# Performance work log

Measured on AMD Instinct MI355X. Metric: run time of the kernel, lower is better.

The kernel has to match this reference:

```python
import jax, jax.numpy as jnp
import numpy as np

C = 32          # mid_channel / in_channel
B = 8           # batch size (number of scenes)
N = 2_000_000   # total points across batch
BN_EPS = 1e-4   # BatchNorm1d eps from norm_fn


def setup_inputs() -> dict:
    key = jax.random.key(0)
    ks = jax.random.split(key, 8)
    s = 0.05
    return {
        "feats": jax.random.normal(ks[0], (N, C), dtype=jnp.float32),
        "batch_idxs": jnp.sort(jax.random.randint(ks[1], (N,), 0, B, dtype=jnp.int32)),
        "off_w1": jax.random.normal(ks[2], (C, C), dtype=jnp.float32) * s,
        "off_b1": jnp.zeros((C,), jnp.float32),
        "bn_gamma": jnp.ones((C,), jnp.float32),   # set_bn_init fills 1.0
        "bn_beta": jnp.zeros((C,), jnp.float32),   # set_bn_init fills 0.0
        "off_w2": jax.random.normal(ks[3], (C, 3), dtype=jnp.float32) * s,
        "off_b2": jnp.zeros((3,), jnp.float32),
        "mask_w1": jax.random.normal(ks[4], (C, C), dtype=jnp.float32) * s,
        "mask_b1": jnp.zeros((C,), jnp.float32),
        "mask_w2": jax.random.normal(ks[5], (C, 1), dtype=jnp.float32) * s,
        "mask_b2": jnp.zeros((1,), jnp.float32),
        "iou_w": jax.random.normal(ks[6], (C, 1), dtype=jnp.float32) * s,
        "iou_b": jnp.zeros((1,), jnp.float32),
    }


def reference(feats, batch_idxs, off_w1, off_b1, bn_gamma, bn_beta, off_w2, off_b2,
              mask_w1, mask_b1, mask_w2, mask_b2, iou_w, iou_b):
    # offset_linear = MLP([C, C, 3], norm_fn=BatchNorm1d): Linear -> BN -> ReLU -> Linear
    h = feats @ off_w1 + off_b1                      # [N, C]
    mu = h.mean(axis=0)
    var = jnp.mean(jnp.square(h - mu), axis=0)       # biased var (torch BN training fwd)
    h = (h - mu) * jax.lax.rsqrt(var + BN_EPS) * bn_gamma + bn_beta
    h = jax.nn.relu(h)
    pt_offsets = h @ off_w2 + off_b2                 # [N, 3]

    # mask_linear = MLP([C, C, 1], norm_fn=None): Linear -> ReLU -> Linear
    m = jax.nn.relu(feats @ mask_w1 + mask_b1)       # [N, C]
    mask_scores = m @ mask_w2 + mask_b2              # [N, 1]

    # global_pool: scatter mean of features over per-batch segments (batch offsets)
    ones = jnp.ones((feats.shape[0],), feats.dtype)
    counts = jax.ops.segment_sum(ones, batch_idxs, num_segments=B)          # [B]
    pooled = jax.ops.segment_sum(feats, batch_idxs, num_segments=B)         # [B, C]
    pooled = pooled / jnp.maximum(counts, 1.0)[:, None]

    # iou_score_linear on the pooled proposal feature
    iou_scores = pooled @ iou_w + iou_b              # [B, 1]
    return pt_offsets, mask_scores, pooled, iou_scores
```

## Files before the change

kernel.cpp:

```cpp
#include <hip/hip_runtime.h>

#define TPB 256
#define NBLK 1024

typedef __attribute__((ext_vector_type(8))) short short8;
typedef __attribute__((ext_vector_type(4))) float floatx4;

__device__ __forceinline__ unsigned short bf_trunc(float f){
    union { float f; unsigned u; } c; c.f = f;
    return (unsigned short)(c.u >> 16);
}
__device__ __forceinline__ unsigned short bf_rne(float f){
    union { float f; unsigned u; } c; c.f = f;
    unsigned r = c.u + 0x7fffu + ((c.u >> 16) & 1u);
    return (unsigned short)(r >> 16);
}

__global__ __launch_bounds__(TPB) void pass1_kernel(
    const float* __restrict__ feats, const int* __restrict__ bidx,
    const float* __restrict__ w1, const float* __restrict__ b1,
    const float* __restrict__ mw1, const float* __restrict__ mb1,
    const float* __restrict__ mw2, const float* __restrict__ mb2,
    float* __restrict__ mask_out,
    float* __restrict__ ws_sum, float* __restrict__ ws_sq,
    float* __restrict__ ws_pool, int N)
{
    __shared__ float s_pool[8][32];
    __shared__ float s_sum[32];
    __shared__ float s_sq[32];

    const int tid = threadIdx.x;
    if (tid < 32){ s_sum[tid] = 0.f; s_sq[tid] = 0.f; }
    ((float*)s_pool)[tid] = 0.f;
    __syncthreads();

    const int lane = tid & 63;
    const int p = lane & 15;
    const int q = lane >> 4;

    short8 aw0, aw1, am0, am1;
    floatx4 ci_h0, ci_h1, ci_m0, ci_m1;
    float mw2v[8];
#pragma unroll
    for (int j = 0; j < 8; ++j){
        const int k = q * 8 + j;
        aw0[j] = (short)bf_rne(w1 [k * 32 + p]);
        aw1[j] = (short)bf_rne(w1 [k * 32 + 16 + p]);
        am0[j] = (short)bf_rne(mw1[k * 32 + p]);
        am1[j] = (short)bf_rne(mw1[k * 32 + 16 + p]);
    }
#pragma unroll
    for (int r = 0; r < 4; ++r){
        const int c0 = q * 4 + r, c1 = 16 + q * 4 + r;
        ci_h0[r] = b1[c0];  ci_h1[r] = b1[c1];
        ci_m0[r] = mb1[c0]; ci_m1[r] = mb1[c1];
        mw2v[r] = mw2[c0];  mw2v[4 + r] = mw2[c1];
    }
    const float mb2s = mb2[0];

    float hsum[8] = {0,0,0,0,0,0,0,0};
    float hsq [8] = {0,0,0,0,0,0,0,0};
    float pacc[8] = {0,0,0,0,0,0,0,0};
    int curb = -1;

    const int  ntiles = (N + 15) >> 4;
    const long nw  = (long)gridDim.x * (TPB / 64);
    const long wid = (long)blockIdx.x * (TPB / 64) + (tid >> 6);
    const int  t0 = (int)(wid * (long)ntiles / nw);
    const int  t1 = (int)((wid + 1) * (long)ntiles / nw);

    for (int t = t0; t < t1; ++t){
        const int row0 = t << 4;
        const int row  = row0 + p;
        const bool valid = (row < N);

        floatx4 v0 = {0.f,0.f,0.f,0.f}, v1 = {0.f,0.f,0.f,0.f};
        if (valid){
            const floatx4* rp = (const floatx4*)(feats + (size_t)row * 32 + q * 8);
            v0 = rp[0]; v1 = rp[1];
        }

        const int b = valid ? bidx[row] : -1;
        if (b != curb){
            if (curb >= 0){
#pragma unroll
                for (int j = 0; j < 8; ++j){
                    atomicAdd(&s_pool[curb][q * 8 + j], pacc[j]);
                    pacc[j] = 0.f;
                }
            }
            curb = b;
        }
        if (b >= 0){
            pacc[0] += v0[0]; pacc[1] += v0[1]; pacc[2] += v0[2]; pacc[3] += v0[3];
            pacc[4] += v1[0]; pacc[5] += v1[1]; pacc[6] += v1[2]; pacc[7] += v1[3];
        }

        short8 bfrag;
        bfrag[0] = (short)bf_trunc(v0[0]); bfrag[1] = (short)bf_trunc(v0[1]);
        bfrag[2] = (short)bf_trunc(v0[2]); bfrag[3] = (short)bf_trunc(v0[3]);
        bfrag[4] = (short)bf_trunc(v1[0]); bfrag[5] = (short)bf_trunc(v1[1]);
        bfrag[6] = (short)bf_trunc(v1[2]); bfrag[7] = (short)bf_trunc(v1[3]);

        const floatx4 ch0 = __builtin_amdgcn_mfma_f32_16x16x32_bf16(aw0, bfrag, ci_h0, 0, 0, 0);
        const floatx4 ch1 = __builtin_amdgcn_mfma_f32_16x16x32_bf16(aw1, bfrag, ci_h1, 0, 0, 0);
        const floatx4 cm0 = __builtin_amdgcn_mfma_f32_16x16x32_bf16(am0, bfrag, ci_m0, 0, 0, 0);
        const floatx4 cm1 = __builtin_amdgcn_mfma_f32_16x16x32_bf16(am1, bfrag, ci_m1, 0, 0, 0);

        if (valid){
#pragma unroll
            for (int r = 0; r < 4; ++r){
                const float h0 = ch0[r]; hsum[r]     += h0; hsq[r]     = fmaf(h0, h0, hsq[r]);
                const float h1 = ch1[r]; hsum[4 + r] += h1; hsq[4 + r] = fmaf(h1, h1, hsq[4 + r]);
            }
        }

        float tm = 0.f;
#pragma unroll
        for (int r = 0; r < 4; ++r){
            tm = fmaf(fmaxf(cm0[r], 0.f), mw2v[r],     tm);
            tm = fmaf(fmaxf(cm1[r], 0.f), mw2v[4 + r], tm);
        }
        tm += __shfl_xor(tm, 16, 64);
        tm += __shfl_xor(tm, 32, 64);
        if (q == 0 && valid) mask_out[row] = tm + mb2s;
    }

    if (curb >= 0){
#pragma unroll
        for (int j = 0; j < 8; ++j) atomicAdd(&s_pool[curb][q * 8 + j], pacc[j]);
    }
#pragma unroll
    for (int i = 0; i < 8; ++i){
        const int ch = (i >> 2) * 16 + q * 4 + (i & 3);
        atomicAdd(&s_sum[ch], hsum[i]);
        atomicAdd(&s_sq[ch],  hsq[i]);
    }
    __syncthreads();
    if (tid < 32){
        atomicAdd(&ws_sum[tid], s_sum[tid]);
        atomicAdd(&ws_sq[tid],  s_sq[tid]);
    }
    {
        const float pv = ((float*)s_pool)[tid];
        if (pv != 0.f) atomicAdd(&ws_pool[tid], pv);
    }
}

__global__ __launch_bounds__(TPB) void finalize_kernel(
    const int* __restrict__ bidx,
    const float* __restrict__ gamma, const float* __restrict__ beta,
    const float* __restrict__ w1, const float* __restrict__ b1,
    const float* __restrict__ iw, const float* __restrict__ ib,
    const float* __restrict__ ws_sum, const float* __restrict__ ws_sq,
    const float* __restrict__ ws_pool,
    float* __restrict__ ws_w1f, float* __restrict__ ws_b1f,
    float* __restrict__ pooled_out, float* __restrict__ iou_out,
    int N, int B)
{
    __shared__ float s_s[32];
    __shared__ float s_pooled[256];
    __shared__ int   s_lb[33];

    const int tid = threadIdx.x;
    if (tid <= B){
        int lo = 0, hi = N;
        while (lo < hi){
            const int mid = (lo + hi) >> 1;
            if (bidx[mid] < tid) lo = mid + 1; else hi = mid;
        }
        s_lb[tid] = lo;
    }
    if (tid < 32){
        const float invN = 1.f / (float)N;
        const float mu  = ws_sum[tid] * invN;
        const float var = ws_sq[tid] * invN - mu * mu;
        const float s   = gamma[tid] * rsqrtf(var + 1e-4f);
        s_s[tid] = s;
        ws_b1f[tid] = (b1[tid] - mu) * s + beta[tid];
    }
    __syncthreads();
    for (int idx = tid; idx < 1024; idx += TPB)
        ws_w1f[idx] = w1[idx] * s_s[idx & 31];
    if (tid < B * 32){
        const int b = tid >> 5;
        const float cnt = fmaxf((float)(s_lb[b + 1] - s_lb[b]), 1.f);
        const float p = ws_pool[tid] / cnt;
        s_pooled[tid]   = p;
        pooled_out[tid] = p;
    }
    __syncthreads();
    if (tid < B){
        float acc = ib[0];
#pragma unroll
        for (int i = 0; i < 32; ++i) acc = fmaf(s_pooled[tid * 32 + i], iw[i], acc);
        iou_out[tid] = acc;
    }
}

__global__ __launch_bounds__(TPB) void pass2_kernel(
    const float* __restrict__ feats,
    const float* __restrict__ ws_w1f, const float* __restrict__ ws_b1f,
    const float* __restrict__ w2, const float* __restrict__ b2,
    float* __restrict__ pt_out, int N)
{
    const int tid = threadIdx.x;
    const int lane = tid & 63;
    const int p = lane & 15;
    const int q = lane >> 4;

    short8 aw0, aw1;
    floatx4 ci0, ci1;
    float w2v[24];
    float b2v0, b2v1, b2v2;
#pragma unroll
    for (int j = 0; j < 8; ++j){
        const int k = q * 8 + j;
        aw0[j] = (short)bf_rne(ws_w1f[k * 32 + p]);
        aw1[j] = (short)bf_rne(ws_w1f[k * 32 + 16 + p]);
    }
#pragma unroll
    for (int r = 0; r < 4; ++r){
        ci0[r] = ws_b1f[q * 4 + r];
        ci1[r] = ws_b1f[16 + q * 4 + r];
    }
#pragma unroll
    for (int i = 0; i < 8; ++i){
        const int ch = (i >> 2) * 16 + q * 4 + (i & 3);
        w2v[i]      = w2[ch * 3 + 0];
        w2v[8 + i]  = w2[ch * 3 + 1];
        w2v[16 + i] = w2[ch * 3 + 2];
    }
    b2v0 = b2[0]; b2v1 = b2[1]; b2v2 = b2[2];

    const int  ntiles = (N + 15) >> 4;
    const long nw  = (long)gridDim.x * (TPB / 64);
    const long wid = (long)blockIdx.x * (TPB / 64) + (tid >> 6);
    const int  t0 = (int)(wid * (long)ntiles / nw);
    const int  t1 = (int)((wid + 1) * (long)ntiles / nw);

    for (int t = t0; t < t1; ++t){
        const int row0 = t << 4;
        const int row  = row0 + p;
        const bool valid = (row < N);

        floatx4 v0 = {0.f,0.f,0.f,0.f}, v1 = {0.f,0.f,0.f,0.f};
        if (valid){
            const floatx4* rp = (const floatx4*)(feats + (size_t)row * 32 + q * 8);
            v0 = rp[0]; v1 = rp[1];
        }
        short8 bfrag;
        bfrag[0] = (short)bf_trunc(v0[0]); bfrag[1] = (short)bf_trunc(v0[1]);
        bfrag[2] = (short)bf_trunc(v0[2]); bfrag[3] = (short)bf_trunc(v0[3]);
        bfrag[4] = (short)bf_trunc(v1[0]); bfrag[5] = (short)bf_trunc(v1[1]);
        bfrag[6] = (short)bf_trunc(v1[2]); bfrag[7] = (short)bf_trunc(v1[3]);

        const floatx4 c0 = __builtin_amdgcn_mfma_f32_16x16x32_bf16(aw0, bfrag, ci0, 0, 0, 0);
        const floatx4 c1 = __builtin_amdgcn_mfma_f32_16x16x32_bf16(aw1, bfrag, ci1, 0, 0, 0);

        float s0 = 0.f, s1 = 0.f, s2 = 0.f;
#pragma unroll
        for (int r = 0; r < 4; ++r){
            const float p0 = fmaxf(c0[r], 0.f);
            const float p1 = fmaxf(c1[r], 0.f);
            s0 = fmaf(p0, w2v[r],          s0); s0 = fmaf(p1, w2v[4 + r],      s0);
            s1 = fmaf(p0, w2v[8 + r],      s1); s1 = fmaf(p1, w2v[12 + r],     s1);
            s2 = fmaf(p0, w2v[16 + r],     s2); s2 = fmaf(p1, w2v[20 + r],     s2);
        }
        s0 += __shfl_xor(s0, 16, 64); s0 += __shfl_xor(s0, 32, 64);
        s1 += __shfl_xor(s1, 16, 64); s1 += __shfl_xor(s1, 32, 64);
        s2 += __shfl_xor(s2, 16, 64); s2 += __shfl_xor(s2, 32, 64);

        if (lane < 48 && valid){
            float val = (q == 0) ? (s0 + b2v0) : ((q == 1) ? (s1 + b2v1) : (s2 + b2v2));
            pt_out[(size_t)row0 * 3 + p * 3 + q] = val;
        }
    }
}

extern "C" void kernel_launch(void* const* d_in, const int* in_sizes, int n_in,
                              void* d_out, int out_size, void* d_ws, size_t ws_size,
                              hipStream_t stream) {
    const float* feats = (const float*)d_in[0];
    const int*   bidx  = (const int*)d_in[1];
    const float* w1    = (const float*)d_in[2];
    const float* b1    = (const float*)d_in[3];
    const float* gamma = (const float*)d_in[4];
    const float* beta  = (const float*)d_in[5];
    const float* w2    = (const float*)d_in[6];
    const float* b2    = (const float*)d_in[7];
    const float* mw1   = (const float*)d_in[8];
    const float* mb1   = (const float*)d_in[9];
    const float* mw2   = (const float*)d_in[10];
    const float* mb2   = (const float*)d_in[11];
    const float* iw    = (const float*)d_in[12];
    const float* ib    = (const float*)d_in[13];

    const int N = in_sizes[0] / 32;
    const int B = (out_size - 4 * N) / 33;

    float* out    = (float*)d_out;
    float* pt     = out;
    float* mask   = out + (size_t)3 * N;
    float* pooled = out + (size_t)4 * N;
    float* iou    = pooled + (size_t)B * 32;

    float* ws      = (float*)d_ws;
    float* ws_sum  = ws;
    float* ws_sq   = ws + 32;
    float* ws_pool = ws + 64;
    float* ws_b1f  = ws + 64 + B * 32;
    float* ws_w1f  = ws + 96 + B * 32;

    hipMemsetAsync(ws, 0, (size_t)(64 + B * 32) * sizeof(float), stream);

    pass1_kernel<<<NBLK, TPB, 0, stream>>>(feats, bidx, w1, b1, mw1, mb1, mw2, mb2,
                                           mask, ws_sum, ws_sq, ws_pool, N);
    finalize_kernel<<<1, TPB, 0, stream>>>(bidx, gamma, beta, w1, b1, iw, ib,
                                           ws_sum, ws_sq, ws_pool,
                                           ws_w1f, ws_b1f, pooled, iou, N, B);
    pass2_kernel<<<NBLK, TPB, 0, stream>>>(feats, ws_w1f, ws_b1f, w2, b2, pt, N);
}
```

Measured before the change: 474.8 us.

## Fuse three passes into one cooperative kernel with grid-wide sync

```diff
diff --git a/kernel.cpp b/kernel.cpp
--- a/kernel.cpp
+++ b/kernel.cpp
@@ -1,7 +1,10 @@
 #include <hip/hip_runtime.h>
+#include <hip/hip_cooperative_groups.h>
+
+namespace cg = cooperative_groups;
 
 #define TPB 256
-#define NBLK 1024
+#define MAXBLK 1024
 
 typedef __attribute__((ext_vector_type(8))) short short8;
 typedef __attribute__((ext_vector_type(4))) float floatx4;
@@ -16,47 +19,59 @@
     return (unsigned short)(r >> 16);
 }
 
-__global__ __launch_bounds__(TPB) void pass1_kernel(
-    const float* __restrict__ feats, const int* __restrict__ bidx,
-    const float* __restrict__ w1, const float* __restrict__ b1,
-    const float* __restrict__ mw1, const float* __restrict__ mb1,
-    const float* __restrict__ mw2, const float* __restrict__ mb2,
-    float* __restrict__ mask_out,
-    float* __restrict__ ws_sum, float* __restrict__ ws_sq,
-    float* __restrict__ ws_pool, int N)
+struct Params {
+    const float* feats; const int* bidx;
+    const float* w1; const float* b1;
+    const float* gamma; const float* beta;
+    const float* w2; const float* b2;
+    const float* mw1; const float* mb1;
+    const float* mw2; const float* mb2;
+    const float* iw; const float* ib;
+    float* pt; float* mask; float* pooled; float* iou;
+    float* ws_sum; float* ws_sq; float* ws_pool;
+    int N; int B;
+};
+
+__global__ __launch_bounds__(TPB, 4) void inst_head_fused(Params P)
 {
     __shared__ float s_pool[8][32];
     __shared__ float s_sum[32];
     __shared__ float s_sq[32];
-
-    const int tid = threadIdx.x;
+    __shared__ float s_sc[32];
+    __shared__ float s_bp[32];
+    __shared__ float s_pooled[256];
+    __shared__ int   s_lb[33];
+
+    const int tid  = threadIdx.x;
+    const int lane = tid & 63;
+    const int p = lane & 15;
+    const int q = lane >> 4;
+
+    const int N = P.N, B = P.B;
+
     if (tid < 32){ s_sum[tid] = 0.f; s_sq[tid] = 0.f; }
     ((float*)s_pool)[tid] = 0.f;
     __syncthreads();
 
-    const int lane = tid & 63;
-    const int p = lane & 15;
-    const int q = lane >> 4;
-
     short8 aw0, aw1, am0, am1;
     floatx4 ci_h0, ci_h1, ci_m0, ci_m1;
     float mw2v[8];
 #pragma unroll
     for (int j = 0; j < 8; ++j){
         const int k = q * 8 + j;
-        aw0[j] = (short)bf_rne(w1 [k * 32 + p]);
-        aw1[j] = (short)bf_rne(w1 [k * 32 + 16 + p]);
-        am0[j] = (short)bf_rne(mw1[k * 32 + p]);
-        am1[j] = (short)bf_rne(mw1[k * 32 + 16 + p]);
+        aw0[j] = (short)bf_rne(P.w1 [k * 32 + p]);
+        aw1[j] = (short)bf_rne(P.w1 [k * 32 + 16 + p]);
+        am0[j] = (short)bf_rne(P.mw1[k * 32 + p]);
+        am1[j] = (short)bf_rne(P.mw1[k * 32 + 16 + p]);
     }
 #pragma unroll
     for (int r = 0; r < 4; ++r){
         const int c0 = q * 4 + r, c1 = 16 + q * 4 + r;
-        ci_h0[r] = b1[c0];  ci_h1[r] = b1[c1];
-        ci_m0[r] = mb1[c0]; ci_m1[r] = mb1[c1];
-        mw2v[r] = mw2[c0];  mw2v[4 + r] = mw2[c1];
-    }
-    const float mb2s = mb2[0];
+        ci_h0[r] = P.b1[c0];  ci_h1[r] = P.b1[c1];
+        ci_m0[r] = P.mb1[c0]; ci_m1[r] = P.mb1[c1];
+        mw2v[r] = P.mw2[c0];  mw2v[4 + r] = P.mw2[c1];
+    }
+    const float mb2s = P.mb2[0];
 
     float hsum[8] = {0,0,0,0,0,0,0,0};
     float hsq [8] = {0,0,0,0,0,0,0,0};
@@ -76,11 +91,11 @@
 
         floatx4 v0 = {0.f,0.f,0.f,0.f}, v1 = {0.f,0.f,0.f,0.f};
         if (valid){
-            const floatx4* rp = (const floatx4*)(feats + (size_t)row * 32 + q * 8);
+            const floatx4* rp = (const floatx4*)(P.feats + (size_t)row * 32 + q * 8);
             v0 = rp[0]; v1 = rp[1];
         }
 
-        const int b = valid ? bidx[row] : -1;
+        const int b = valid ? P.bidx[row] : -1;
         if (b != curb){
             if (curb >= 0){
 #pragma unroll
@@ -123,7 +138,7 @@
         }
         tm += __shfl_xor(tm, 16, 64);
         tm += __shfl_xor(tm, 32, 64);
-        if (q == 0 && valid) mask_out[row] = tm + mb2s;
+        if (q == 0 && valid) P.mask[row] = tm + mb2s;
     }
 
     if (curb >= 0){
@@ -138,106 +153,75 @@
     }
     __syncthreads();
     if (tid < 32){
-        atomicAdd(&ws_sum[tid], s_sum[tid]);
-        atomicAdd(&ws_sq[tid],  s_sq[tid]);
+        atomicAdd(&P.ws_sum[tid], s_sum[tid]);
+        atomicAdd(&P.ws_sq[tid],  s_sq[tid]);
     }
     {
         const float pv = ((float*)s_pool)[tid];
-        if (pv != 0.f) atomicAdd(&ws_pool[tid], pv);
-    }
-}
-
-__global__ __launch_bounds__(TPB) void finalize_kernel(
-    const int* __restrict__ bidx,
-    const float* __restrict__ gamma, const float* __restrict__ beta,
-    const float* __restrict__ w1, const float* __restrict__ b1,
-    const float* __restrict__ iw, const float* __restrict__ ib,
-    const float* __restrict__ ws_sum, const float* __restrict__ ws_sq,
-    const float* __restrict__ ws_pool,
-    float* __restrict__ ws_w1f, float* __restrict__ ws_b1f,
-    float* __restrict__ pooled_out, float* __restrict__ iou_out,
-    int N, int B)
-{
-    __shared__ float s_s[32];
-    __shared__ float s_pooled[256];
-    __shared__ int   s_lb[33];
-
-    const int tid = threadIdx.x;
-    if (tid <= B){
-        int lo = 0, hi = N;
-        while (lo < hi){
-            const int mid = (lo + hi) >> 1;
-            if (bidx[mid] < tid) lo = mid + 1; else hi = mid;
-        }
-        s_lb[tid] = lo;
-    }
+        if (pv != 0.f) atomicAdd(&P.ws_pool[tid], pv);
+    }
+
+    cg::this_grid().sync();
+
+    if (blockIdx.x == 0){
+        if (tid <= B){
+            int lo = 0, hi = N;
+            while (lo < hi){
+                const int mid = (lo + hi) >> 1;
+                if (P.bidx[mid] < tid) lo = mid + 1; else hi = mid;
+            }
+            s_lb[tid] = lo;
+        }
+        __syncthreads();
+        if (tid < B * 32){
+            const int bb = tid >> 5;
+            const float cnt = fmaxf((float)(s_lb[bb + 1] - s_lb[bb]), 1.f);
+            const float pv = P.ws_pool[tid] / cnt;
+            s_pooled[tid] = pv;
+            P.pooled[tid] = pv;
+        }
+        __syncthreads();
+        if (tid < B){
+            float acc = P.ib[0];
+#pragma unroll
+            for (int i = 0; i < 32; ++i) acc = fmaf(s_pooled[tid * 32 + i], P.iw[i], acc);
+            P.iou[tid] = acc;
+        }
+    }
+
     if (tid < 32){
         const float invN = 1.f / (float)N;
-        const float mu  = ws_sum[tid] * invN;
-        const float var = ws_sq[tid] * invN - mu * mu;
-        const float s   = gamma[tid] * rsqrtf(var + 1e-4f);
-        s_s[tid] = s;
-        ws_b1f[tid] = (b1[tid] - mu) * s + beta[tid];
+        const float mu  = P.ws_sum[tid] * invN;
+        const float var = P.ws_sq[tid] * invN - mu * mu;
+        const float s   = P.gamma[tid] * rsqrtf(var + 1e-4f);
+        s_sc[tid] = s;
+        s_bp[tid] = (P.b1[tid] - mu) * s + P.beta[tid];
     }
     __syncthreads();
-    for (int idx = tid; idx < 1024; idx += TPB)
-        ws_w1f[idx] = w1[idx] * s_s[idx & 31];
-    if (tid < B * 32){
-        const int b = tid >> 5;
-        const float cnt = fmaxf((float)(s_lb[b + 1] - s_lb[b]), 1.f);
-        const float p = ws_pool[tid] / cnt;
-        s_pooled[tid]   = p;
-        pooled_out[tid] = p;
-    }
-    __syncthreads();
-    if (tid < B){
-        float acc = ib[0];
-#pragma unroll
-        for (int i = 0; i < 32; ++i) acc = fmaf(s_pooled[tid * 32 + i], iw[i], acc);
-        iou_out[tid] = acc;
-    }
-}
-
-__global__ __launch_bounds__(TPB) void pass2_kernel(
-    const float* __restrict__ feats,
-    const float* __restrict__ ws_w1f, const float* __restrict__ ws_b1f,
-    const float* __restrict__ w2, const float* __restrict__ b2,
-    float* __restrict__ pt_out, int N)
-{
-    const int tid = threadIdx.x;
-    const int lane = tid & 63;
-    const int p = lane & 15;
-    const int q = lane >> 4;
-
-    short8 aw0, aw1;
-    floatx4 ci0, ci1;
+
+    short8 pw0, pw1;
+    floatx4 pc0, pc1;
     float w2v[24];
-    float b2v0, b2v1, b2v2;
+    const float sc0 = s_sc[p], sc1 = s_sc[16 + p];
 #pragma unroll
     for (int j = 0; j < 8; ++j){
         const int k = q * 8 + j;
-        aw0[j] = (short)bf_rne(ws_w1f[k * 32 + p]);
-        aw1[j] = (short)bf_rne(ws_w1f[k * 32 + 16 + p]);
+        pw0[j] = (short)bf_rne(P.w1[k * 32 + p]      * sc0);
+        pw1[j] = (short)bf_rne(P.w1[k * 32 + 16 + p] * sc1);
     }
 #pragma unroll
     for (int r = 0; r < 4; ++r){
-        ci0[r] = ws_b1f[q * 4 + r];
-        ci1[r] = ws_b1f[16 + q * 4 + r];
+        pc0[r] = s_bp[q * 4 + r];
+        pc1[r] = s_bp[16 + q * 4 + r];
     }
 #pragma unroll
     for (int i = 0; i < 8; ++i){
         const int ch = (i >> 2) * 16 + q * 4 + (i & 3);
-        w2v[i]      = w2[ch * 3 + 0];
-        w2v[8 + i]  = w2[ch * 3 + 1];
-        w2v[16 + i] = w2[ch * 3 + 2];
-    }
-    b2v0 = b2[0]; b2v1 = b2[1]; b2v2 = b2[2];
-
-    const int  ntiles = (N + 15) >> 4;
-    const long nw  = (long)gridDim.x * (TPB / 64);
-    const long wid = (long)blockIdx.x * (TPB / 64) + (tid >> 6);
-    const int  t0 = (int)(wid * (long)ntiles / nw);
-    const int  t1 = (int)((wid + 1) * (long)ntiles / nw);
+        w2v[i]      = P.w2[ch * 3 + 0];
+        w2v[8 + i]  = P.w2[ch * 3 + 1];
+        w2v[16 + i] = P.w2[ch * 3 + 2];
+    }
+    const float b2v0 = P.b2[0], b2v1 = P.b2[1], b2v2 = P.b2[2];
 
     for (int t = t0; t < t1; ++t){
         const int row0 = t << 4;
@@ -246,7 +230,7 @@
 
         floatx4 v0 = {0.f,0.f,0.f,0.f}, v1 = {0.f,0.f,0.f,0.f};
         if (valid){
-            const floatx4* rp = (const floatx4*)(feats + (size_t)row * 32 + q * 8);
+            const floatx4* rp = (const floatx4*)(P.feats + (size_t)row * 32 + q * 8);
             v0 = rp[0]; v1 = rp[1];
         }
         short8 bfrag;
@@ -255,17 +239,17 @@
         bfrag[4] = (short)bf_trunc(v1[0]); bfrag[5] = (short)bf_trunc(v1[1]);
         bfrag[6] = (short)bf_trunc(v1[2]); bfrag[7] = (short)bf_trunc(v1[3]);
 
-        const floatx4 c0 = __builtin_amdgcn_mfma_f32_16x16x32_bf16(aw0, bfrag, ci0, 0, 0, 0);
-        const floatx4 c1 = __builtin_amdgcn_mfma_f32_16x16x32_bf16(aw1, bfrag, ci1, 0, 0, 0);
+        const floatx4 c0 = __builtin_amdgcn_mfma_f32_16x16x32_bf16(pw0, bfrag, pc0, 0, 0, 0);
+        const floatx4 c1 = __builtin_amdgcn_mfma_f32_16x16x32_bf16(pw1, bfrag, pc1, 0, 0, 0);
 
         float s0 = 0.f, s1 = 0.f, s2 = 0.f;
 #pragma unroll
         for (int r = 0; r < 4; ++r){
             const float p0 = fmaxf(c0[r], 0.f);
             const float p1 = fmaxf(c1[r], 0.f);
-            s0 = fmaf(p0, w2v[r],          s0); s0 = fmaf(p1, w2v[4 + r],      s0);
-            s1 = fmaf(p0, w2v[8 + r],      s1); s1 = fmaf(p1, w2v[12 + r],     s1);
-            s2 = fmaf(p0, w2v[16 + r],     s2); s2 = fmaf(p1, w2v[20 + r],     s2);
+            s0 = fmaf(p0, w2v[r],      s0); s0 = fmaf(p1, w2v[4 + r],  s0);
+            s1 = fmaf(p0, w2v[8 + r],  s1); s1 = fmaf(p1, w2v[12 + r], s1);
+            s2 = fmaf(p0, w2v[16 + r], s2); s2 = fmaf(p1, w2v[20 + r], s2);
         }
         s0 += __shfl_xor(s0, 16, 64); s0 += __shfl_xor(s0, 32, 64);
         s1 += __shfl_xor(s1, 16, 64); s1 += __shfl_xor(s1, 32, 64);
@@ -273,7 +257,7 @@
 
         if (lane < 48 && valid){
             float val = (q == 0) ? (s0 + b2v0) : ((q == 1) ? (s1 + b2v1) : (s2 + b2v2));
-            pt_out[(size_t)row0 * 3 + p * 3 + q] = val;
+            P.pt[(size_t)row0 * 3 + p * 3 + q] = val;
         }
     }
 }
@@ -281,43 +265,50 @@
 extern "C" void kernel_launch(void* const* d_in, const int* in_sizes, int n_in,
                               void* d_out, int out_size, void* d_ws, size_t ws_size,
                               hipStream_t stream) {
-    const float* feats = (const float*)d_in[0];
-    const int*   bidx  = (const int*)d_in[1];
-    const float* w1    = (const float*)d_in[2];
-    const float* b1    = (const float*)d_in[3];
-    const float* gamma = (const float*)d_in[4];
-    const float* beta  = (const float*)d_in[5];
-    const float* w2    = (const float*)d_in[6];
-    const float* b2    = (const float*)d_in[7];
-    const float* mw1   = (const float*)d_in[8];
-    const float* mb1   = (const float*)d_in[9];
-    const float* mw2   = (const float*)d_in[10];
-    const float* mb2   = (const float*)d_in[11];
-    const float* iw    = (const float*)d_in[12];
-    const float* ib    = (const float*)d_in[13];
+    Params P;
+    P.feats = (const float*)d_in[0];
+    P.bidx  = (const int*)d_in[1];
+    P.w1    = (const float*)d_in[2];
+    P.b1    = (const float*)d_in[3];
+    P.gamma = (const float*)d_in[4];
+    P.beta  = (const float*)d_in[5];
+    P.w2    = (const float*)d_in[6];
+    P.b2    = (const float*)d_in[7];
+    P.mw1   = (const float*)d_in[8];
+    P.mb1   = (const float*)d_in[9];
+    P.mw2   = (const float*)d_in[10];
+    P.mb2   = (const float*)d_in[11];
+    P.iw    = (const float*)d_in[12];
+    P.ib    = (const float*)d_in[13];
 
     const int N = in_sizes[0] / 32;
     const int B = (out_size - 4 * N) / 33;
-
-    float* out    = (float*)d_out;
-    float* pt     = out;
-    float* mask   = out + (size_t)3 * N;
-    float* pooled = out + (size_t)4 * N;
-    float* iou    = pooled + (size_t)B * 32;
-
-    float* ws      = (float*)d_ws;
-    float* ws_sum  = ws;
-    float* ws_sq   = ws + 32;
-    float* ws_pool = ws + 64;
-    float* ws_b1f  = ws + 64 + B * 32;
-    float* ws_w1f  = ws + 96 + B * 32;
+    P.N = N; P.B = B;
+
+    float* out = (float*)d_out;
+    P.pt     = out;
+    P.mask   = out + (size_t)3 * N;
+    P.pooled = out + (size_t)4 * N;
+    P.iou    = P.pooled + (size_t)B * 32;
+
+    float* ws = (float*)d_ws;
+    P.ws_sum  = ws;
+    P.ws_sq   = ws + 32;
+    P.ws_pool = ws + 64;
 
     hipMemsetAsync(ws, 0, (size_t)(64 + B * 32) * sizeof(float), stream);
 
-    pass1_kernel<<<NBLK, TPB, 0, stream>>>(feats, bidx, w1, b1, mw1, mb1, mw2, mb2,
-                                           mask, ws_sum, ws_sq, ws_pool, N);
-    finalize_kernel<<<1, TPB, 0, stream>>>(bidx, gamma, beta, w1, b1, iw, ib,
-                                           ws_sum, ws_sq, ws_pool,
-                                           ws_w1f, ws_b1f, pooled, iou, N, B);
-    pass2_kernel<<<NBLK, TPB, 0, stream>>>(feats, ws_w1f, ws_b1f, w2, b2, pt, N);
+    int dev = 0;
+    hipGetDevice(&dev);
+    hipDeviceProp_t prop;
+    hipGetDeviceProperties(&prop, dev);
+    int perCU = 0;
+    hipOccupancyMaxActiveBlocksPerMultiprocessor(&perCU, inst_head_fused, TPB, 0);
+    int grid = perCU * prop.multiProcessorCount;
+    if (grid > MAXBLK) grid = MAXBLK;
+    if (grid < 1) grid = 1;
+
+    void* args[] = { (void*)&P };
+    hipLaunchCooperativeKernel((const void*)inst_head_fused,
+                               dim3(grid), dim3(TPB), args, 0, stream);
 }
```

Measured after the change: 528.4 us. 1.11x slower.

## Fold finalize into pass2, software-prefetch next tile, retune grid sizes

Applied to the files above, without the earlier changes.

```diff
diff --git a/kernel.cpp b/kernel.cpp
--- a/kernel.cpp
+++ b/kernel.cpp
@@ -1,7 +1,6 @@
 #include <hip/hip_runtime.h>
 
 #define TPB 256
-#define NBLK 1024
 
 typedef __attribute__((ext_vector_type(8))) short short8;
 typedef __attribute__((ext_vector_type(4))) float floatx4;
@@ -16,7 +15,7 @@
     return (unsigned short)(r >> 16);
 }
 
-__global__ __launch_bounds__(TPB) void pass1_kernel(
+__global__ __launch_bounds__(TPB, 7) void pass1_kernel(
     const float* __restrict__ feats, const int* __restrict__ bidx,
     const float* __restrict__ w1, const float* __restrict__ b1,
     const float* __restrict__ mw1, const float* __restrict__ mb1,
@@ -29,14 +28,14 @@
     __shared__ float s_sum[32];
     __shared__ float s_sq[32];
 
-    const int tid = threadIdx.x;
+    const int tid  = threadIdx.x;
+    const int lane = tid & 63;
+    const int p = lane & 15;
+    const int q = lane >> 4;
+
     if (tid < 32){ s_sum[tid] = 0.f; s_sq[tid] = 0.f; }
     ((float*)s_pool)[tid] = 0.f;
     __syncthreads();
-
-    const int lane = tid & 63;
-    const int p = lane & 15;
-    const int q = lane >> 4;
 
     short8 aw0, aw1, am0, am1;
     floatx4 ci_h0, ci_h1, ci_m0, ci_m1;
@@ -69,18 +68,30 @@
     const int  t0 = (int)(wid * (long)ntiles / nw);
     const int  t1 = (int)((wid + 1) * (long)ntiles / nw);
 
-    for (int t = t0; t < t1; ++t){
-        const int row0 = t << 4;
-        const int row  = row0 + p;
-        const bool valid = (row < N);
-
-        floatx4 v0 = {0.f,0.f,0.f,0.f}, v1 = {0.f,0.f,0.f,0.f};
-        if (valid){
+    floatx4 v0 = {0.f,0.f,0.f,0.f}, v1 = {0.f,0.f,0.f,0.f};
+    int b = -1;
+    if (t0 < t1){
+        const int row = (t0 << 4) + p;
+        if (row < N){
             const floatx4* rp = (const floatx4*)(feats + (size_t)row * 32 + q * 8);
             v0 = rp[0]; v1 = rp[1];
-        }
-
-        const int b = valid ? bidx[row] : -1;
+            b  = bidx[row];
+        }
+    }
+
+    for (int t = t0; t < t1; ++t){
+        floatx4 nv0 = {0.f,0.f,0.f,0.f}, nv1 = {0.f,0.f,0.f,0.f};
+        int nb = -1;
+        if (t + 1 < t1){
+            const int nrow = ((t + 1) << 4) + p;
+            if (nrow < N){
+                const floatx4* rp = (const floatx4*)(feats + (size_t)nrow * 32 + q * 8);
+                nv0 = rp[0]; nv1 = rp[1];
+                nb  = bidx[nrow];
+            }
+        }
+
+        const bool valid = (b >= 0);
         if (b != curb){
             if (curb >= 0){
 #pragma unroll
@@ -91,7 +102,7 @@
             }
             curb = b;
         }
-        if (b >= 0){
+        if (valid){
             pacc[0] += v0[0]; pacc[1] += v0[1]; pacc[2] += v0[2]; pacc[3] += v0[3];
             pacc[4] += v1[0]; pacc[5] += v1[1]; pacc[6] += v1[2]; pacc[7] += v1[3];
         }
@@ -123,7 +134,9 @@
         }
         tm += __shfl_xor(tm, 16, 64);
         tm += __shfl_xor(tm, 32, 64);
-        if (q == 0 && valid) mask_out[row] = tm + mb2s;
+        if (q == 0 && valid) mask_out[(t << 4) + p] = tm + mb2s;
+
+        v0 = nv0; v1 = nv1; b = nb;
     }
 
     if (curb >= 0){
@@ -147,82 +160,77 @@
     }
 }
 
-__global__ __launch_bounds__(TPB) void finalize_kernel(
-    const int* __restrict__ bidx,
+__global__ __launch_bounds__(TPB, 6) void pass2_kernel(
+    const float* __restrict__ feats, const int* __restrict__ bidx,
+    const float* __restrict__ w1, const float* __restrict__ b1,
     const float* __restrict__ gamma, const float* __restrict__ beta,
-    const float* __restrict__ w1, const float* __restrict__ b1,
+    const float* __restrict__ w2, const float* __restrict__ b2,
     const float* __restrict__ iw, const float* __restrict__ ib,
     const float* __restrict__ ws_sum, const float* __restrict__ ws_sq,
     const float* __restrict__ ws_pool,
-    float* __restrict__ ws_w1f, float* __restrict__ ws_b1f,
-    float* __restrict__ pooled_out, float* __restrict__ iou_out,
-    int N, int B)
+    float* __restrict__ pt_out, float* __restrict__ pooled_out,
+    float* __restrict__ iou_out, int N, int B)
 {
-    __shared__ float s_s[32];
+    __shared__ float s_sc[32];
+    __shared__ float s_bp[32];
     __shared__ float s_pooled[256];
     __shared__ int   s_lb[33];
 
-    const int tid = threadIdx.x;
-    if (tid <= B){
-        int lo = 0, hi = N;
-        while (lo < hi){
-            const int mid = (lo + hi) >> 1;
-            if (bidx[mid] < tid) lo = mid + 1; else hi = mid;
-        }
-        s_lb[tid] = lo;
-    }
+    const int tid  = threadIdx.x;
+    const int lane = tid & 63;
+    const int p = lane & 15;
+    const int q = lane >> 4;
+
     if (tid < 32){
         const float invN = 1.f / (float)N;
         const float mu  = ws_sum[tid] * invN;
         const float var = ws_sq[tid] * invN - mu * mu;
         const float s   = gamma[tid] * rsqrtf(var + 1e-4f);
-        s_s[tid] = s;
-        ws_b1f[tid] = (b1[tid] - mu) * s + beta[tid];
+        s_sc[tid] = s;
+        s_bp[tid] = (b1[tid] - mu) * s + beta[tid];
     }
     __syncthreads();
-    for (int idx = tid; idx < 1024; idx += TPB)
-        ws_w1f[idx] = w1[idx] * s_s[idx & 31];
-    if (tid < B * 32){
-        const int b = tid >> 5;
-        const float cnt = fmaxf((float)(s_lb[b + 1] - s_lb[b]), 1.f);
-        const float p = ws_pool[tid] / cnt;
-        s_pooled[tid]   = p;
-        pooled_out[tid] = p;
-    }
-    __syncthreads();
-    if (tid < B){
-        float acc = ib[0];
-#pragma unroll
-        for (int i = 0; i < 32; ++i) acc = fmaf(s_pooled[tid * 32 + i], iw[i], acc);
-        iou_out[tid] = acc;
-    }
-}
-
-__global__ __launch_bounds__(TPB) void pass2_kernel(
-    const float* __restrict__ feats,
-    const float* __restrict__ ws_w1f, const float* __restrict__ ws_b1f,
-    const float* __restrict__ w2, const float* __restrict__ b2,
-    float* __restrict__ pt_out, int N)
-{
-    const int tid = threadIdx.x;
-    const int lane = tid & 63;
-    const int p = lane & 15;
-    const int q = lane >> 4;
-
-    short8 aw0, aw1;
-    floatx4 ci0, ci1;
+
+    if (blockIdx.x == 0){
+        if (tid <= B){
+            int lo = 0, hi = N;
+            while (lo < hi){
+                const int mid = (lo + hi) >> 1;
+                if (bidx[mid] < tid) lo = mid + 1; else hi = mid;
+            }
+            s_lb[tid] = lo;
+        }
+        __syncthreads();
+        if (tid < B * 32){
+            const int bb = tid >> 5;
+            const float cnt = fmaxf((float)(s_lb[bb + 1] - s_lb[bb]), 1.f);
+            const float pv = ws_pool[tid] / cnt;
+            s_pooled[tid]   = pv;
+            pooled_out[tid] = pv;
+        }
+        __syncthreads();
+        if (tid < B){
+            float acc = ib[0];
+#pragma unroll
+            for (int i = 0; i < 32; ++i) acc = fmaf(s_pooled[tid * 32 + i], iw[i], acc);
+            iou_out[tid] = acc;
+        }
+    }
+
+    short8 pw0, pw1;
+    floatx4 pc0, pc1;
     float w2v[24];
-    float b2v0, b2v1, b2v2;
+    const float sc0 = s_sc[p], sc1 = s_sc[16 + p];
 #pragma unroll
     for (int j = 0; j < 8; ++j){
         const int k = q * 8 + j;
-        aw0[j] = (short)bf_rne(ws_w1f[k * 32 + p]);
-        aw1[j] = (short)bf_rne(ws_w1f[k * 32 + 16 + p]);
+        pw0[j] = (short)bf_rne(w1[k * 32 + p]      * sc0);
+        pw1[j] = (short)bf_rne(w1[k * 32 + 16 + p] * sc1);
     }
 #pragma unroll
     for (int r = 0; r < 4; ++r){
-        ci0[r] = ws_b1f[q * 4 + r];
-        ci1[r] = ws_b1f[16 + q * 4 + r];
+        pc0[r] = s_bp[q * 4 + r];
+        pc1[r] = s_bp[16 + q * 4 + r];
     }
 #pragma unroll
     for (int i = 0; i < 8; ++i){
@@ -231,7 +239,7 @@
         w2v[8 + i]  = w2[ch * 3 + 1];
         w2v[16 + i] = w2[ch * 3 + 2];
     }
-    b2v0 = b2[0]; b2v1 = b2[1]; b2v2 = b2[2];
+    const float b2v0 = b2[0], b2v1 = b2[1], b2v2 = b2[2];
 
     const int  ntiles = (N + 15) >> 4;
     const long nw  = (long)gridDim.x * (TPB / 64);
@@ -239,33 +247,46 @@
     const int  t0 = (int)(wid * (long)ntiles / nw);
     const int  t1 = (int)((wid + 1) * (long)ntiles / nw);
 
-    for (int t = t0; t < t1; ++t){
-        const int row0 = t << 4;
-        const int row  = row0 + p;
-        const bool valid = (row < N);
-
-        floatx4 v0 = {0.f,0.f,0.f,0.f}, v1 = {0.f,0.f,0.f,0.f};
-        if (valid){
+    floatx4 v0 = {0.f,0.f,0.f,0.f}, v1 = {0.f,0.f,0.f,0.f};
+    bool valid = false;
+    if (t0 < t1){
+        const int row = (t0 << 4) + p;
+        if (row < N){
             const floatx4* rp = (const floatx4*)(feats + (size_t)row * 32 + q * 8);
             v0 = rp[0]; v1 = rp[1];
-        }
+            valid = true;
+        }
+    }
+
+    for (int t = t0; t < t1; ++t){
+        floatx4 nv0 = {0.f,0.f,0.f,0.f}, nv1 = {0.f,0.f,0.f,0.f};
+        bool nvalid = false;
+        if (t + 1 < t1){
+            const int nrow = ((t + 1) << 4) + p;
+            if (nrow < N){
+                const floatx4* rp = (const floatx4*)(feats + (size_t)nrow * 32 + q * 8);
+                nv0 = rp[0]; nv1 = rp[1];
+                nvalid = true;
+            }
+        }
+
         short8 bfrag;
         bfrag[0] = (short)bf_trunc(v0[0]); bfrag[1] = (short)bf_trunc(v0[1]);
         bfrag[2] = (short)bf_trunc(v0[2]); bfrag[3] = (short)bf_trunc(v0[3]);
         bfrag[4] = (short)bf_trunc(v1[0]); bfrag[5] = (short)bf_trunc(v1[1]);
         bfrag[6] = (short)bf_trunc(v1[2]); bfrag[7] = (short)bf_trunc(v1[3]);
 
-        const floatx4 c0 = __builtin_amdgcn_mfma_f32_16x16x32_bf16(aw0, bfrag, ci0, 0, 0, 0);
-        const floatx4 c1 = __builtin_amdgcn_mfma_f32_16x16x32_bf16(aw1, bfrag, ci1, 0, 0, 0);
+        const floatx4 c0 = __builtin_amdgcn_mfma_f32_16x16x32_bf16(pw0, bfrag, pc0, 0, 0, 0);
+        const floatx4 c1 = __builtin_amdgcn_mfma_f32_16x16x32_bf16(pw1, bfrag, pc1, 0, 0, 0);
 
         float s0 = 0.f, s1 = 0.f, s2 = 0.f;
 #pragma unroll
         for (int r = 0; r < 4; ++r){
             const float p0 = fmaxf(c0[r], 0.f);
             const float p1 = fmaxf(c1[r], 0.f);
-            s0 = fmaf(p0, w2v[r],          s0); s0 = fmaf(p1, w2v[4 + r],      s0);
-            s1 = fmaf(p0, w2v[8 + r],      s1); s1 = fmaf(p1, w2v[12 + r],     s1);
-            s2 = fmaf(p0, w2v[16 + r],     s2); s2 = fmaf(p1, w2v[20 + r],     s2);
+            s0 = fmaf(p0, w2v[r],      s0); s0 = fmaf(p1, w2v[4 + r],  s0);
+            s1 = fmaf(p0, w2v[8 + r],  s1); s1 = fmaf(p1, w2v[12 + r], s1);
+            s2 = fmaf(p0, w2v[16 + r], s2); s2 = fmaf(p1, w2v[20 + r], s2);
         }
         s0 += __shfl_xor(s0, 16, 64); s0 += __shfl_xor(s0, 32, 64);
         s1 += __shfl_xor(s1, 16, 64); s1 += __shfl_xor(s1, 32, 64);
@@ -273,8 +294,10 @@
 
         if (lane < 48 && valid){
             float val = (q == 0) ? (s0 + b2v0) : ((q == 1) ? (s1 + b2v1) : (s2 + b2v2));
-            pt_out[(size_t)row0 * 3 + p * 3 + q] = val;
-        }
+            pt_out[(size_t)(t << 4) * 3 + p * 3 + q] = val;
+        }
+
+        v0 = nv0; v1 = nv1; valid = nvalid;
     }
 }
 
@@ -309,15 +332,12 @@
     float* ws_sum  = ws;
     float* ws_sq   = ws + 32;
     float* ws_pool = ws + 64;
-    float* ws_b1f  = ws + 64 + B * 32;
-    float* ws_w1f  = ws + 96 + B * 32;
 
     hipMemsetAsync(ws, 0, (size_t)(64 + B * 32) * sizeof(float), stream);
 
-    pass1_kernel<<<NBLK, TPB, 0, stream>>>(feats, bidx, w1, b1, mw1, mb1, mw2, mb2,
+    pass1_kernel<<<1792, TPB, 0, stream>>>(feats, bidx, w1, b1, mw1, mb1, mw2, mb2,
                                            mask, ws_sum, ws_sq, ws_pool, N);
-    finalize_kernel<<<1, TPB, 0, stream>>>(bidx, gamma, beta, w1, b1, iw, ib,
-                                           ws_sum, ws_sq, ws_pool,
-                                           ws_w1f, ws_b1f, pooled, iou, N, B);
-    pass2_kernel<<<NBLK, TPB, 0, stream>>>(feats, ws_w1f, ws_b1f, w2, b2, pt, N);
-}
+    pass2_kernel<<<1536, TPB, 0, stream>>>(feats, bidx, w1, b1, gamma, beta, w2, b2,
+                                           iw, ib, ws_sum, ws_sq, ws_pool,
+                                           pt, pooled, iou, N, B);
+}
```

Result: slower. 694.7 us (+46.3%).
